# Optimization experiments

Hardware: AMD Instinct MI355X
Metric: run time of the kernel (lower is better)

## Reference

```python
import jax, jax.numpy as jnp
import numpy as np


def gcn_layer(h, src, dst, norm, W, b, num_nodes):
    # PyG GCNConv: linear transform, normalized scatter-add aggregation, then bias
    h = h @ W                                    # [N, out]
    msg = h[src] * norm[:, None]                 # [E+N, out] gathered messages
    out = jax.ops.segment_sum(msg, dst, num_segments=num_nodes)
    return out + b


def setup_inputs() -> dict:
    key = jax.random.key(0)
    ks = jax.random.split(key, 6)
    N, E, D, H, C = 100000, 1600000, 128, 64, 2
    x = jax.random.normal(ks[0], (N, D), dtype=jnp.float32)
    edge_index = jax.random.randint(ks[1], (2, E), 0, N, dtype=jnp.int64)
    def glorot(k, shape):
        lim = np.sqrt(6.0 / (shape[0] + shape[1]))
        return jax.random.uniform(k, shape, jnp.float32, -lim, lim)
    return {
        "x": x,
        "edge_index": edge_index,
        "W1": glorot(ks[2], (D, H)), "b1": jnp.zeros((H,), jnp.float32),
        "W2": glorot(ks[3], (H, H)), "b2": jnp.zeros((H,), jnp.float32),
        "W3": glorot(ks[4], (H, H)), "b3": jnp.zeros((H,), jnp.float32),
        "Wfc": glorot(ks[5], (H, C)), "bfc": jnp.zeros((C,), jnp.float32),
    }


def reference(x, edge_index, W1, b1, W2, b2, W3, b3, Wfc, bfc):
    N = x.shape[0]
    # add self loops (GCNConv default), symmetric deg^-1/2 normalization
    loops = jnp.arange(N, dtype=edge_index.dtype)
    src = jnp.concatenate([edge_index[0], loops])
    dst = jnp.concatenate([edge_index[1], loops])
    deg = jax.ops.segment_sum(jnp.ones_like(dst, dtype=x.dtype), dst, num_segments=N)
    dinv = jnp.where(deg > 0, jax.lax.rsqrt(deg), 0.0)
    norm = dinv[src] * dinv[dst]

    h = jax.nn.relu(gcn_layer(x, src, dst, norm, W1, b1, N))
    h = jax.nn.relu(gcn_layer(h, src, dst, norm, W2, b2, N))
    h = jax.nn.relu(gcn_layer(h, src, dst, norm, W3, b3, N))
    logits = h @ Wfc + bfc
    return jax.nn.log_softmax(logits, axis=1)
```

## Files before the change

kernel.cpp:

```cpp
#include <hip/hip_runtime.h>
#include <math.h>


static inline size_t alignup(size_t x){ return (x + 511) & ~size_t(511); }

typedef float v4f __attribute__((ext_vector_type(4)));
typedef unsigned short v4u16 __attribute__((ext_vector_type(4)));
typedef __attribute__((ext_vector_type(8))) short short8;
typedef __attribute__((ext_vector_type(4))) float f32x4;

__device__ __forceinline__ unsigned short f32_to_bf16(float f){
  union { float f; unsigned int u; } c; c.f = f;
  unsigned int u = c.u + 0x7FFFu + ((c.u >> 16) & 1u);
  return (unsigned short)(u >> 16);
}
__device__ __forceinline__ v4f bf16x4_to_f32(v4u16 a){
  union { unsigned int u; float f; } c0,c1,c2,c3;
  c0.u = (unsigned int)a.x << 16;
  c1.u = (unsigned int)a.y << 16;
  c2.u = (unsigned int)a.z << 16;
  c3.u = (unsigned int)a.w << 16;
  v4f r; r.x=c0.f; r.y=c1.f; r.z=c2.f; r.w=c3.f;
  return r;
}

#define NBUCK 1024
#define CHUNK 8192
#define CCAP  3584

__global__ void zero_kernel(int* __restrict__ p, int n){
  int i = blockIdx.x*256 + threadIdx.x;
  if(i<n) p[i] = 0;
}

__global__ void wfrag_kernel(const float* __restrict__ W,
                             unsigned short* __restrict__ wf, int ksteps){
  int t = threadIdx.x + blockIdx.x*256;
  int total = ksteps*4*64;
  if(t >= total) return;
  int l  = t & 63;
  int nb = (t>>6) & 3;
  int ks = t>>8;
  int k0 = ks*32 + 8*(l>>4);
  int n  = nb*16 + (l&15);
  unsigned short* o = wf + (size_t)t*8;
  #pragma unroll
  for(int i=0;i<8;i++) o[i] = f32_to_bf16(W[(size_t)(k0+i)*64 + n]);
}

__global__ __launch_bounds__(1024) void hist_kernel(const int* __restrict__ dst,
                                                    int* __restrict__ bcnt, int E){
  __shared__ int h[NBUCK];
  int t = threadIdx.x;
  h[t]=0;
  __syncthreads();
  int base = blockIdx.x*CHUNK;
  #pragma unroll
  for(int i=0;i<CHUNK;i+=1024){
    int e = base+i+t;
    if(e<E) atomicAdd(&h[dst[e]>>7], 1);
  }
  __syncthreads();
  if(h[t]) atomicAdd(&bcnt[t], h[t]);
}

__global__ void scan_buckets_kernel(const int* __restrict__ bcnt, int* __restrict__ bbase,
                                    int* __restrict__ bfill){
  __shared__ int sh[256];
  int t = threadIdx.x;
  int v0=bcnt[4*t], v1=bcnt[4*t+1], v2=bcnt[4*t+2], v3=bcnt[4*t+3];
  int ts = v0+v1+v2+v3;
  sh[t]=ts; __syncthreads();
  for(int off=1; off<256; off<<=1){
    int x=(t>=off)?sh[t-off]:0; __syncthreads();
    sh[t]+=x; __syncthreads();
  }
  int run = sh[t]-ts;
  int i0=4*t;
  bbase[i0+0]=run; bfill[i0+0]=run; run+=v0;
  bbase[i0+1]=run; bfill[i0+1]=run; run+=v1;
  bbase[i0+2]=run; bfill[i0+2]=run; run+=v2;
  bbase[i0+3]=run; bfill[i0+3]=run;
}

__global__ __launch_bounds__(1024) void scatter_kernel(const int* __restrict__ src,
                                                       const int* __restrict__ dst,
                                                       int* __restrict__ bfill,
                                                       int* __restrict__ pairs, int E){
  __shared__ int hist[NBUCK];
  __shared__ int delta[NBUCK];
  __shared__ int wsum[16];
  __shared__ int vals[CHUNK];
  __shared__ unsigned short bkt[CHUNK];
  int t = threadIdx.x;
  int lane = t & 63, wid = t >> 6;
  int cbase = blockIdx.x*CHUNK;
  hist[t]=0;
  __syncthreads();
  #pragma unroll
  for(int i=0;i<CHUNK;i+=1024){
    int e = cbase+i+t;
    if(e<E) atomicAdd(&hist[dst[e]>>7], 1);
  }
  __syncthreads();
  int v = hist[t];
  int x = v;
  #pragma unroll
  for(int off=1; off<64; off<<=1){
    int y = __shfl_up(x, off, 64);
    if(lane >= off) x += y;
  }
  if(lane==63) wsum[wid]=x;
  __syncthreads();
  if(wid==0){
    int s2 = (lane<16) ? wsum[lane] : 0;
    #pragma unroll
    for(int off=1; off<16; off<<=1){
      int y = __shfl_up(s2, off, 64);
      if(lane >= off) s2 += y;
    }
    if(lane<16) wsum[lane]=s2;
  }
  __syncthreads();
  int run = (x - v) + (wid ? wsum[wid-1] : 0);
  int g = v ? atomicAdd(&bfill[t], v) : 0;
  hist[t]=run; delta[t]=g-run;
  __syncthreads();
  #pragma unroll
  for(int i=0;i<CHUNK;i+=1024){
    int e = cbase+i+t;
    if(e<E){
      int d = dst[e];
      int b = d>>7;
      int slot = atomicAdd(&hist[b], 1);
      vals[slot] = ((d&127)<<17) | src[e];
      bkt[slot]  = (unsigned short)b;
    }
  }
  __syncthreads();
  int cnt = E - cbase; if(cnt > CHUNK) cnt = CHUNK;
  for(int i=t;i<cnt;i+=1024){
    int b = bkt[i];
    pairs[delta[b] + i] = vals[i];
  }
}

__global__ __launch_bounds__(256) void bucket_csr_kernel(const int* __restrict__ pairs,
                                                         const int* __restrict__ bbase,
                                                         int* __restrict__ row_ptr,
                                                         float* __restrict__ dinv,
                                                         int* __restrict__ col,
                                                         int N, int E){
  __shared__ int hist[128];
  __shared__ int pref[128];
  __shared__ int fill[128];
  __shared__ int srcs[CCAP];
  int b = blockIdx.x, t = threadIdx.x;
  int s = bbase[b], e = bbase[b+1];
  int cnt = e - s; if(cnt > CCAP) cnt = CCAP;
  if(t<128) hist[t]=0;
  __syncthreads();
  int v[CCAP/256];
  #pragma unroll
  for(int i=0;i<CCAP/256;i++){
    int idx = i*256 + t;
    if(idx<cnt){ v[i]=pairs[s+idx]; atomicAdd(&hist[v[i]>>17], 1); }
  }
  __syncthreads();
  if(t<128) pref[t]=hist[t];
  __syncthreads();
  for(int off=1; off<128; off<<=1){
    int x=0;
    if(t<128 && t>=off) x=pref[t-off];
    __syncthreads();
    if(t<128) pref[t]+=x;
    __syncthreads();
  }
  if(t<128){
    int ex = pref[t]-hist[t];
    fill[t]=ex;
    int node = b*128 + t;
    if(node<N){
      row_ptr[node] = s + ex;
      dinv[node] = rsqrtf((float)(hist[t]+1));
    }
  }
  if(b==0 && t==0) row_ptr[N]=E;
  __syncthreads();
  #pragma unroll
  for(int i=0;i<CCAP/256;i++){
    int idx = i*256 + t;
    if(idx<cnt){
      int ld = v[i]>>17;
      int pos = atomicAdd(&fill[ld], 1);
      srcs[pos] = v[i] & 0x1FFFF;
    }
  }
  __syncthreads();
  for(int i=t;i<cnt;i+=256) col[s+i]=srcs[i];
}

__global__ __launch_bounds__(256) void lin_mfma_kernel(const float* __restrict__ x,
                                                       const unsigned short* __restrict__ wf,
                                                       const float* __restrict__ dinv,
                                                       unsigned short* __restrict__ g,
                                                       int N){
  __shared__ __align__(16) unsigned short wl[4*4*64*8];
  int t = threadIdx.x, wave = t>>6, lane = t&63;
  #pragma unroll
  for(int idx=t; idx<1024; idx+=256)
    ((v4f*)wl)[idx] = ((const v4f*)wf)[idx];
  __syncthreads();
  int row = blockIdx.x*64 + wave*16 + (lane&15);
  int arow = row < N ? row : N-1;
  const float* xr = x + (size_t)arow*128 + 8*(lane>>4);
  f32x4 acc0={0.f,0.f,0.f,0.f}, acc1=acc0, acc2=acc0, acc3=acc0;
  #pragma unroll
  for(int ks=0; ks<4; ks++){
    v4f a0 = *(const v4f*)(xr + ks*32);
    v4f a1 = *(const v4f*)(xr + ks*32 + 4);
    short8 af;
    af[0]=(short)f32_to_bf16(a0.x); af[1]=(short)f32_to_bf16(a0.y);
    af[2]=(short)f32_to_bf16(a0.z); af[3]=(short)f32_to_bf16(a0.w);
    af[4]=(short)f32_to_bf16(a1.x); af[5]=(short)f32_to_bf16(a1.y);
    af[6]=(short)f32_to_bf16(a1.z); af[7]=(short)f32_to_bf16(a1.w);
    const short8* wb = ((const short8*)wl) + ks*256 + lane;
    acc0 = __builtin_amdgcn_mfma_f32_16x16x32_bf16(af, wb[0],   acc0, 0, 0, 0);
    acc1 = __builtin_amdgcn_mfma_f32_16x16x32_bf16(af, wb[64],  acc1, 0, 0, 0);
    acc2 = __builtin_amdgcn_mfma_f32_16x16x32_bf16(af, wb[128], acc2, 0, 0, 0);
    acc3 = __builtin_amdgcn_mfma_f32_16x16x32_bf16(af, wb[192], acc3, 0, 0, 0);
  }
  int rbase = blockIdx.x*64 + wave*16 + (lane>>4)*4;
  int c = lane & 15;
  #pragma unroll
  for(int j=0;j<4;j++){
    int r = rbase + j;
    if(r < N){
      float dv = dinv[r];
      unsigned short* go = g + (size_t)r*64 + c;
      go[0]  = f32_to_bf16(dv*acc0[j]);
      go[16] = f32_to_bf16(dv*acc1[j]);
      go[32] = f32_to_bf16(dv*acc2[j]);
      go[48] = f32_to_bf16(dv*acc3[j]);
    }
  }
}

__device__ __forceinline__ v4f gather_row4(const unsigned short* __restrict__ g,
                                           const int* __restrict__ col,
                                           int n, int s, int e, int l, int ZR){
  v4f acc = bf16x4_to_f32(*(const v4u16*)&g[(size_t)n*64 + l*4]);
  for(int i = s; i < e; i += 16){
    int rem = e - i;
    int myc = (l < rem) ? col[i + l] : ZR;
    #pragma unroll
    for(int j0 = 0; j0 < 16; j0 += 4){
      int c0 = __shfl(myc, j0+0, 16);
      int c1 = __shfl(myc, j0+1, 16);
      int c2 = __shfl(myc, j0+2, 16);
      int c3 = __shfl(myc, j0+3, 16);
      v4f x0 = bf16x4_to_f32(*(const v4u16*)&g[(size_t)c0*64 + l*4]);
      v4f x1 = bf16x4_to_f32(*(const v4u16*)&g[(size_t)c1*64 + l*4]);
      v4f x2 = bf16x4_to_f32(*(const v4u16*)&g[(size_t)c2*64 + l*4]);
      v4f x3 = bf16x4_to_f32(*(const v4u16*)&g[(size_t)c3*64 + l*4]);
      acc = acc + ((x0 + x1) + (x2 + x3));
      if(j0+4 >= rem) break;
    }
  }
  return acc;
}

__global__ __launch_bounds__(256) void agg_lin_kernel(const unsigned short* __restrict__ g,
                                                      const int* __restrict__ row_ptr,
                                                      const int* __restrict__ col,
                                                      const float* __restrict__ dinv,
                                                      const float* __restrict__ bias,
                                                      const unsigned short* __restrict__ wf,
                                                      unsigned short* __restrict__ g2,
                                                      int N){
  __shared__ __align__(16) unsigned short hsh[16*72];
  __shared__ __align__(16) unsigned short wl[2*4*64*8];
  int t = threadIdx.x, wave = t>>6, lane = t&63;
  int l = lane & 15, q = lane >> 4;
  #pragma unroll
  for(int idx = t; idx < 512; idx += 256)
    ((v4f*)wl)[idx] = ((const v4f*)wf)[idx];
  int base = blockIdx.x*16;
  int n = base + wave*4 + q;
  bool valid = n < N;
  int nn = valid ? n : (N-1);
  int s = row_ptr[nn], e = row_ptr[nn+1];
  v4f acc = gather_row4(g, col, nn, s, e, l, N);
  float dv = dinv[nn];
  v4f bs = *(const v4f*)&bias[l*4];
  v4u16 hb;
  hb.x = f32_to_bf16(fmaxf(fmaf(dv, acc.x, bs.x), 0.f));
  hb.y = f32_to_bf16(fmaxf(fmaf(dv, acc.y, bs.y), 0.f));
  hb.z = f32_to_bf16(fmaxf(fmaf(dv, acc.z, bs.z), 0.f));
  hb.w = f32_to_bf16(fmaxf(fmaf(dv, acc.w, bs.w), 0.f));
  *(v4u16*)&hsh[(wave*4+q)*72 + l*4] = hb;
  __syncthreads();
  short8 a0 = *(const short8*)&hsh[(lane&15)*72 +      8*(lane>>4)];
  short8 a1 = *(const short8*)&hsh[(lane&15)*72 + 32 + 8*(lane>>4)];
  const short8* wb = ((const short8*)wl) + wave*64 + lane;
  f32x4 oc = {0.f,0.f,0.f,0.f};
  oc = __builtin_amdgcn_mfma_f32_16x16x32_bf16(a0, wb[0],   oc, 0, 0, 0);
  oc = __builtin_amdgcn_mfma_f32_16x16x32_bf16(a1, wb[256], oc, 0, 0, 0);
  int c  = wave*16 + (lane&15);
  int r0 = base + (lane>>4)*4;
  #pragma unroll
  for(int j=0;j<4;j++){
    int r = r0 + j;
    if(r < N)
      g2[(size_t)r*64 + c] = f32_to_bf16(dinv[r]*oc[j]);
  }
}

__global__ __launch_bounds__(256) void agg_final_kernel(const unsigned short* __restrict__ g,
                                                        const int* __restrict__ row_ptr,
                                                        const int* __restrict__ col,
                                                        const float* __restrict__ dinv,
                                                        const float* __restrict__ bias,
                                                        const float* __restrict__ Wfc,
                                                        const float* __restrict__ bfc,
                                                        float* __restrict__ out, int N){
  int t = threadIdx.x, wave = t>>6, lane = t&63;
  int l = lane & 15, q = lane >> 4;
  int n = blockIdx.x*16 + wave*4 + q;
  bool valid = n < N;
  if(!valid) n = N-1;
  int s = row_ptr[n], e = row_ptr[n+1];
  v4f acc = gather_row4(g, col, n, s, e, l, N);
  float dv = dinv[n];
  v4f bs = *(const v4f*)&bias[l*4];
  v4f hv;
  hv.x = fmaxf(fmaf(dv, acc.x, bs.x), 0.f);
  hv.y = fmaxf(fmaf(dv, acc.y, bs.y), 0.f);
  hv.z = fmaxf(fmaf(dv, acc.z, bs.z), 0.f);
  hv.w = fmaxf(fmaf(dv, acc.w, bs.w), 0.f);
  v4f wa = *(const v4f*)&Wfc[l*8];
  v4f wb = *(const v4f*)&Wfc[l*8+4];
  float p0 = hv.x*wa.x + hv.y*wa.z + hv.z*wb.x + hv.w*wb.z;
  float p1 = hv.x*wa.y + hv.y*wa.w + hv.z*wb.y + hv.w*wb.w;
  for(int off=8; off; off>>=1){
    p0 += __shfl_down(p0, off, 16);
    p1 += __shfl_down(p1, off, 16);
  }
  if(valid && l==0){
    float l0 = p0 + bfc[0], l1 = p1 + bfc[1];
    float m  = fmaxf(l0, l1);
    float lse = m + logf(expf(l0-m) + expf(l1-m));
    out[(size_t)n*2+0] = l0 - lse;
    out[(size_t)n*2+1] = l1 - lse;
  }
}

extern "C" void kernel_launch(void* const* d_in, const int* in_sizes, int n_in,
                              void* d_out, int out_size, void* d_ws, size_t ws_size,
                              hipStream_t stream) {
  (void)n_in; (void)out_size; (void)ws_size;
  const float* x   = (const float*)d_in[0];
  const int*   ei  = (const int*)  d_in[1];
  const float* W1  = (const float*)d_in[2];
  const float* b1  = (const float*)d_in[3];
  const float* W2  = (const float*)d_in[4];
  const float* b2  = (const float*)d_in[5];
  const float* W3  = (const float*)d_in[6];
  const float* b3  = (const float*)d_in[7];
  const float* Wfc = (const float*)d_in[8];
  const float* bfc = (const float*)d_in[9];
  float* out = (float*)d_out;

  const int N = in_sizes[0] / 128;
  const int E = in_sizes[1] / 2;
  const int* src = ei;
  const int* dst = ei + E;
  const int NB = (N + 127) / 128;

  char* w = (char*)d_ws;
  int*   bcnt    = (int*)  w; w += alignup((size_t)NBUCK*4);
  int*   bbase   = (int*)  w; w += alignup((size_t)(NBUCK+1)*4);
  int*   bfill   = (int*)  w; w += alignup((size_t)NBUCK*4);
  int*   pairs   = (int*)  w; w += alignup((size_t)E*4);
  int*   row_ptr = (int*)  w; w += alignup((size_t)(N+1)*4);
  float* dinv    = (float*)w; w += alignup((size_t)N*4);
  int*   col     = (int*)  w; w += alignup((size_t)E*4);
  unsigned short* gA = (unsigned short*)w; w += alignup((size_t)(N+1)*64*2);
  unsigned short* gB = (unsigned short*)w; w += alignup((size_t)(N+1)*64*2);
  unsigned short* wf1 = (unsigned short*)w; w += alignup((size_t)4*4*64*8*2);
  unsigned short* wf2 = (unsigned short*)w; w += alignup((size_t)2*4*64*8*2);
  unsigned short* wf3 = (unsigned short*)w; w += alignup((size_t)2*4*64*8*2);

  const int nblkE   = (E + CHUNK - 1) / CHUNK;
  const int nblkLin = (N + 63) / 64;
  const int nblkAgg = (N + 15) / 16;

  zero_kernel<<<(NBUCK+255)/256, 256, 0, stream>>>(bcnt, NBUCK);
  zero_kernel<<<1, 256, 0, stream>>>((int*)(gA + (size_t)N*64), 32);
  zero_kernel<<<1, 256, 0, stream>>>((int*)(gB + (size_t)N*64), 32);
  wfrag_kernel<<<4, 256, 0, stream>>>(W1, wf1, 4);
  wfrag_kernel<<<2, 256, 0, stream>>>(W2, wf2, 2);
  wfrag_kernel<<<2, 256, 0, stream>>>(W3, wf3, 2);

  hist_kernel<<<nblkE, 1024, 0, stream>>>(dst, bcnt, E);
  scan_buckets_kernel<<<1, 256, 0, stream>>>(bcnt, bbase, bfill);
  scatter_kernel<<<nblkE, 1024, 0, stream>>>(src, dst, bfill, pairs, E);
  bucket_csr_kernel<<<NB, 256, 0, stream>>>(pairs, bbase, row_ptr, dinv, col, N, E);

  lin_mfma_kernel<<<nblkLin, 256, 0, stream>>>(x, wf1, dinv, gA, N);
  agg_lin_kernel<<<nblkAgg, 256, 0, stream>>>(gA, row_ptr, col, dinv, b1, wf2, gB, N);
  agg_lin_kernel<<<nblkAgg, 256, 0, stream>>>(gB, row_ptr, col, dinv, b2, wf3, gA, N);
  agg_final_kernel<<<nblkAgg, 256, 0, stream>>>(gA, row_ptr, col, dinv, b3,
                                                Wfc, bfc, out, N);
}
```

Before: 251.1 us.

## Replace histogram+scan with fixed-capacity bucket slots and fuse setup kernels

Drops the edge histogram pass and the bucket prefix-scan by giving each destination bucket a fixed CCAP-sized slot in the pairs/col arrays, with bfill counting from zero. Rows are stored as (start,end) int2 pairs instead of a row_ptr array. The zeroing and weight-fragment kernels are merged into one setup kernel, which cuts the launch count. In exchange, one full read of dst and two small launches go away. The risk is that a bucket holding more than CCAP edges would overflow into the next bucket's slot, since the scatter writes without checking capacity.

```diff
diff --git a/kernel.cpp b/kernel.cpp
--- a/kernel.cpp
+++ b/kernel.cpp
@@ -28,59 +28,37 @@
 #define CHUNK 8192
 #define CCAP  3584
 
-__global__ void zero_kernel(int* __restrict__ p, int n){
-  int i = blockIdx.x*256 + threadIdx.x;
-  if(i<n) p[i] = 0;
-}
-
-__global__ void wfrag_kernel(const float* __restrict__ W,
-                             unsigned short* __restrict__ wf, int ksteps){
-  int t = threadIdx.x + blockIdx.x*256;
+__device__ __forceinline__ void wfrag_one(const float* __restrict__ W,
+                                          unsigned short* __restrict__ wf,
+                                          int idx, int ksteps){
   int total = ksteps*4*64;
-  if(t >= total) return;
-  int l  = t & 63;
-  int nb = (t>>6) & 3;
-  int ks = t>>8;
+  if(idx >= total) return;
+  int l  = idx & 63;
+  int nb = (idx>>6) & 3;
+  int ks = idx>>8;
   int k0 = ks*32 + 8*(l>>4);
   int n  = nb*16 + (l&15);
-  unsigned short* o = wf + (size_t)t*8;
+  unsigned short* o = wf + (size_t)idx*8;
   #pragma unroll
   for(int i=0;i<8;i++) o[i] = f32_to_bf16(W[(size_t)(k0+i)*64 + n]);
 }
 
-__global__ __launch_bounds__(1024) void hist_kernel(const int* __restrict__ dst,
-                                                    int* __restrict__ bcnt, int E){
-  __shared__ int h[NBUCK];
-  int t = threadIdx.x;
-  h[t]=0;
-  __syncthreads();
-  int base = blockIdx.x*CHUNK;
-  #pragma unroll
-  for(int i=0;i<CHUNK;i+=1024){
-    int e = base+i+t;
-    if(e<E) atomicAdd(&h[dst[e]>>7], 1);
-  }
-  __syncthreads();
-  if(h[t]) atomicAdd(&bcnt[t], h[t]);
-}
-
-__global__ void scan_buckets_kernel(const int* __restrict__ bcnt, int* __restrict__ bbase,
-                                    int* __restrict__ bfill){
-  __shared__ int sh[256];
-  int t = threadIdx.x;
-  int v0=bcnt[4*t], v1=bcnt[4*t+1], v2=bcnt[4*t+2], v3=bcnt[4*t+3];
-  int ts = v0+v1+v2+v3;
-  sh[t]=ts; __syncthreads();
-  for(int off=1; off<256; off<<=1){
-    int x=(t>=off)?sh[t-off]:0; __syncthreads();
-    sh[t]+=x; __syncthreads();
-  }
-  int run = sh[t]-ts;
-  int i0=4*t;
-  bbase[i0+0]=run; bfill[i0+0]=run; run+=v0;
-  bbase[i0+1]=run; bfill[i0+1]=run; run+=v1;
-  bbase[i0+2]=run; bfill[i0+2]=run; run+=v2;
-  bbase[i0+3]=run; bfill[i0+3]=run;
+__global__ __launch_bounds__(256) void setup_kernel(const float* __restrict__ W1,
+                                                    const float* __restrict__ W2,
+                                                    const float* __restrict__ W3,
+                                                    unsigned short* __restrict__ wf1,
+                                                    unsigned short* __restrict__ wf2,
+                                                    unsigned short* __restrict__ wf3,
+                                                    int* __restrict__ bfill,
+                                                    unsigned short* __restrict__ gAz,
+                                                    unsigned short* __restrict__ gBz){
+  int b = blockIdx.x, t = threadIdx.x;
+  if(b < 4)      wfrag_one(W1, wf1, b*256+t, 4);
+  else if(b < 6) wfrag_one(W2, wf2, (b-4)*256+t, 2);
+  else           wfrag_one(W3, wf3, (b-6)*256+t, 2);
+  if(b < 4) bfill[b*256+t] = 0;
+  if(b==4 && t<32) ((int*)gAz)[t] = 0;
+  if(b==5 && t<32) ((int*)gBz)[t] = 0;
 }
 
 __global__ __launch_bounds__(1024) void scatter_kernel(const int* __restrict__ src,
@@ -124,7 +102,7 @@
   __syncthreads();
   int run = (x - v) + (wid ? wsum[wid-1] : 0);
   int g = v ? atomicAdd(&bfill[t], v) : 0;
-  hist[t]=run; delta[t]=g-run;
+  hist[t]=run; delta[t]= t*CCAP + g - run;
   __syncthreads();
   #pragma unroll
   for(int i=0;i<CHUNK;i+=1024){
@@ -146,25 +124,25 @@
 }
 
 __global__ __launch_bounds__(256) void bucket_csr_kernel(const int* __restrict__ pairs,
-                                                         const int* __restrict__ bbase,
-                                                         int* __restrict__ row_ptr,
+                                                         const int* __restrict__ bfill,
+                                                         int2* __restrict__ rowse,
                                                          float* __restrict__ dinv,
                                                          int* __restrict__ col,
-                                                         int N, int E){
+                                                         int N){
   __shared__ int hist[128];
   __shared__ int pref[128];
   __shared__ int fill[128];
   __shared__ int srcs[CCAP];
   int b = blockIdx.x, t = threadIdx.x;
-  int s = bbase[b], e = bbase[b+1];
-  int cnt = e - s; if(cnt > CCAP) cnt = CCAP;
+  int s0 = b*CCAP;
+  int cnt = bfill[b]; if(cnt > CCAP) cnt = CCAP;
   if(t<128) hist[t]=0;
   __syncthreads();
   int v[CCAP/256];
   #pragma unroll
   for(int i=0;i<CCAP/256;i++){
     int idx = i*256 + t;
-    if(idx<cnt){ v[i]=pairs[s+idx]; atomicAdd(&hist[v[i]>>17], 1); }
+    if(idx<cnt){ v[i]=pairs[s0+idx]; atomicAdd(&hist[v[i]>>17], 1); }
   }
   __syncthreads();
   if(t<128) pref[t]=hist[t];
@@ -181,11 +159,10 @@
     fill[t]=ex;
     int node = b*128 + t;
     if(node<N){
-      row_ptr[node] = s + ex;
+      rowse[node] = make_int2(s0+ex, s0+ex+hist[t]);
       dinv[node] = rsqrtf((float)(hist[t]+1));
     }
   }
-  if(b==0 && t==0) row_ptr[N]=E;
   __syncthreads();
   #pragma unroll
   for(int i=0;i<CCAP/256;i++){
@@ -197,7 +174,7 @@
     }
   }
   __syncthreads();
-  for(int i=t;i<cnt;i+=256) col[s+i]=srcs[i];
+  for(int i=t;i<cnt;i+=256) col[s0+i]=srcs[i];
 }
 
 __global__ __launch_bounds__(256) void lin_mfma_kernel(const float* __restrict__ x,
@@ -271,7 +248,7 @@
 }
 
 __global__ __launch_bounds__(256) void agg_lin_kernel(const unsigned short* __restrict__ g,
-                                                      const int* __restrict__ row_ptr,
+                                                      const int2* __restrict__ rowse,
                                                       const int* __restrict__ col,
                                                       const float* __restrict__ dinv,
                                                       const float* __restrict__ bias,
@@ -289,8 +266,8 @@
   int n = base + wave*4 + q;
   bool valid = n < N;
   int nn = valid ? n : (N-1);
-  int s = row_ptr[nn], e = row_ptr[nn+1];
-  v4f acc = gather_row4(g, col, nn, s, e, l, N);
+  int2 se = rowse[nn];
+  v4f acc = gather_row4(g, col, nn, se.x, se.y, l, N);
   float dv = dinv[nn];
   v4f bs = *(const v4f*)&bias[l*4];
   v4u16 hb;
@@ -317,7 +294,7 @@
 }
 
 __global__ __launch_bounds__(256) void agg_final_kernel(const unsigned short* __restrict__ g,
-                                                        const int* __restrict__ row_ptr,
+                                                        const int2* __restrict__ rowse,
                                                         const int* __restrict__ col,
                                                         const float* __restrict__ dinv,
                                                         const float* __restrict__ bias,
@@ -329,8 +306,8 @@
   int n = blockIdx.x*16 + wave*4 + q;
   bool valid = n < N;
   if(!valid) n = N-1;
-  int s = row_ptr[n], e = row_ptr[n+1];
-  v4f acc = gather_row4(g, col, n, s, e, l, N);
+  int2 se = rowse[n];
+  v4f acc = gather_row4(g, col, n, se.x, se.y, l, N);
   float dv = dinv[n];
   v4f bs = *(const v4f*)&bias[l*4];
   v4f hv;
@@ -378,13 +355,11 @@
   const int NB = (N + 127) / 128;
 
   char* w = (char*)d_ws;
-  int*   bcnt    = (int*)  w; w += alignup((size_t)NBUCK*4);
-  int*   bbase   = (int*)  w; w += alignup((size_t)(NBUCK+1)*4);
   int*   bfill   = (int*)  w; w += alignup((size_t)NBUCK*4);
-  int*   pairs   = (int*)  w; w += alignup((size_t)E*4);
-  int*   row_ptr = (int*)  w; w += alignup((size_t)(N+1)*4);
+  int*   pairs   = (int*)  w; w += alignup((size_t)NBUCK*CCAP*4);
+  int2*  rowse   = (int2*) w; w += alignup((size_t)N*8);
   float* dinv    = (float*)w; w += alignup((size_t)N*4);
-  int*   col     = (int*)  w; w += alignup((size_t)E*4);
+  int*   col     = (int*)  w; w += alignup((size_t)NBUCK*CCAP*4);
   unsigned short* gA = (unsigned short*)w; w += alignup((size_t)(N+1)*64*2);
   unsigned short* gB = (unsigned short*)w; w += alignup((size_t)(N+1)*64*2);
   unsigned short* wf1 = (unsigned short*)w; w += alignup((size_t)4*4*64*8*2);
@@ -395,21 +370,14 @@
   const int nblkLin = (N + 63) / 64;
   const int nblkAgg = (N + 15) / 16;
 
-  zero_kernel<<<(NBUCK+255)/256, 256, 0, stream>>>(bcnt, NBUCK);
-  zero_kernel<<<1, 256, 0, stream>>>((int*)(gA + (size_t)N*64), 32);
-  zero_kernel<<<1, 256, 0, stream>>>((int*)(gB + (size_t)N*64), 32);
-  wfrag_kernel<<<4, 256, 0, stream>>>(W1, wf1, 4);
-  wfrag_kernel<<<2, 256, 0, stream>>>(W2, wf2, 2);
-  wfrag_kernel<<<2, 256, 0, stream>>>(W3, wf3, 2);
-
-  hist_kernel<<<nblkE, 1024, 0, stream>>>(dst, bcnt, E);
-  scan_buckets_kernel<<<1, 256, 0, stream>>>(bcnt, bbase, bfill);
+  setup_kernel<<<8, 256, 0, stream>>>(W1, W2, W3, wf1, wf2, wf3, bfill,
+                                      gA + (size_t)N*64, gB + (size_t)N*64);
   scatter_kernel<<<nblkE, 1024, 0, stream>>>(src, dst, bfill, pairs, E);
-  bucket_csr_kernel<<<NB, 256, 0, stream>>>(pairs, bbase, row_ptr, dinv, col, N, E);
+  bucket_csr_kernel<<<NB, 256, 0, stream>>>(pairs, bfill, rowse, dinv, col, N);
 
   lin_mfma_kernel<<<nblkLin, 256, 0, stream>>>(x, wf1, dinv, gA, N);
-  agg_lin_kernel<<<nblkAgg, 256, 0, stream>>>(gA, row_ptr, col, dinv, b1, wf2, gB, N);
-  agg_lin_kernel<<<nblkAgg, 256, 0, stream>>>(gB, row_ptr, col, dinv, b2, wf3, gA, N);
-  agg_final_kernel<<<nblkAgg, 256, 0, stream>>>(gA, row_ptr, col, dinv, b3,
+  agg_lin_kernel<<<nblkAgg, 256, 0, stream>>>(gA, rowse, col, dinv, b1, wf2, gB, N);
+  agg_lin_kernel<<<nblkAgg, 256, 0, stream>>>(gB, rowse, col, dinv, b2, wf3, gA, N);
+  agg_final_kernel<<<nblkAgg, 256, 0, stream>>>(gA, rowse, col, dinv, b3,
                                                 Wfc, bfc, out, N);
 }
```

After: 234.6 us (median of 2 runs). -6.6%, faster.
